# Optimization experiments

Hardware: AMD Instinct MI355X
Metric: run time of the kernel (lower is better)

Reference implementation:

```python
import jax, jax.numpy as jnp
import numpy as np

NUM_EDGE_TYPES = 8
HIDDEN = 128
N_NODES = 50000
N_EDGES = 600000


def setup_inputs() -> dict:
    key = jax.random.key(0)
    ks = jax.random.split(key, 10)
    H = HIDDEN
    h = jax.random.normal(ks[0], (N_NODES, H), dtype=jnp.float32)
    edge_index = jax.random.randint(ks[1], (2, N_EDGES), 0, N_NODES, dtype=jnp.int32)
    edge_type = jax.random.randint(ks[2], (N_EDGES,), 0, NUM_EDGE_TYPES + 1, dtype=jnp.int32)
    s = 1.0 / np.sqrt(H)
    W_msg = jax.random.uniform(ks[3], (H, H), jnp.float32, -s, s)
    b_msg = jax.random.uniform(ks[4], (H,), jnp.float32, -s, s)
    edge_embed = jax.random.normal(ks[5], (NUM_EDGE_TYPES + 1, H), dtype=jnp.float32)
    W_ih = jax.random.uniform(ks[6], (3 * H, H), jnp.float32, -s, s)
    W_hh = jax.random.uniform(ks[7], (3 * H, H), jnp.float32, -s, s)
    b_ih = jax.random.uniform(ks[8], (3 * H,), jnp.float32, -s, s)
    b_hh = jax.random.uniform(ks[9], (3 * H,), jnp.float32, -s, s)
    return {"h": h, "edge_index": edge_index, "edge_type": edge_type,
            "num_nodes": N_NODES, "W_msg": W_msg, "b_msg": b_msg,
            "edge_embed": edge_embed, "W_ih": W_ih, "W_hh": W_hh,
            "b_ih": b_ih, "b_hh": b_hh}


def _gru_cell(x, h, W_ih, W_hh, b_ih, b_hh):
    # PyTorch GRUCell: gates ordered (r, z, n)
    H = h.shape[-1]
    gi = x @ W_ih.T + b_ih  # (N, 3H)
    gh = h @ W_hh.T + b_hh
    i_r, i_z, i_n = gi[:, :H], gi[:, H:2 * H], gi[:, 2 * H:]
    h_r, h_z, h_n = gh[:, :H], gh[:, H:2 * H], gh[:, 2 * H:]
    r = jax.nn.sigmoid(i_r + h_r)
    z = jax.nn.sigmoid(i_z + h_z)
    n = jnp.tanh(i_n + r * h_n)
    return (1.0 - z) * n + z * h


def reference(h, edge_index, edge_type, num_nodes, W_msg, b_msg, edge_embed, W_ih, W_hh, b_ih, b_hh):
    src = edge_index[0]
    dst = edge_index[1]
    # gather -> linear -> edge-type embed add
    src_h = h[src] @ W_msg.T + b_msg                      # (E, H)
    emb = edge_embed[jnp.clip(edge_type, 0, NUM_EDGE_TYPES)]  # (E, H)
    msg = src_h + emb
    # scatter-add into per-node message buffer
    messages = jax.ops.segment_sum(msg, dst, num_segments=num_nodes)  # (num_nodes, H)
    h_new = _gru_cell(messages, h[:num_nodes], W_ih, W_hh, b_ih, b_hh)
    result = jnp.zeros_like(h).at[:num_nodes].set(h_new)
    return result
```

## Files before the change

### kernel.cpp

```cpp
#include <hip/hip_runtime.h>
#include <math.h>

#define H 128
typedef unsigned int u32;
typedef unsigned long long u64;
typedef __attribute__((ext_vector_type(8))) short short8;
typedef __attribute__((ext_vector_type(4))) float floatx4;

#define XS_STRIDE 136
#define CS_STRIDE 40
#define CAP 64

__device__ __forceinline__ float sigmoid_f(float x) {
    return 1.0f / (1.0f + __expf(-x));
}
__device__ __forceinline__ float tanh_f(float x) {
    float t = __expf(-2.0f * fabsf(x));
    float r = (1.0f - t) / (1.0f + t);
    return copysignf(r, x);
}
__device__ __forceinline__ unsigned short f2bf(float x) {
    u32 u = __float_as_uint(x);
    return (unsigned short)((u + 0x7fffu + ((u >> 16) & 1u)) >> 16);
}
__device__ __forceinline__ float bf2f(unsigned short s) {
    return __uint_as_float(((u32)s) << 16);
}
__device__ __forceinline__ float bf_lo32(u32 u) { return __uint_as_float(u << 16); }
__device__ __forceinline__ float bf_hi32(u32 u) { return __uint_as_float(u & 0xffff0000u); }

__global__ __launch_bounds__(256) void fused_pre_kernel(
    const float* __restrict__ h, unsigned short* __restrict__ h_b, int total8,
    int* __restrict__ deg, int* __restrict__ ohead, int N,
    const float* __restrict__ Wih, const float* __restrict__ Whh,
    const float* __restrict__ Wm,  const float* __restrict__ emb,
    const float* __restrict__ bm,
    unsigned short* __restrict__ Wcs, unsigned short* __restrict__ Whhs,
    unsigned short* __restrict__ embWs, int HB, int DB)
{
    int b = blockIdx.x;
    if (b < HB) {
        int idx = b * 256 + threadIdx.x;
        if (idx >= total8) return;
        const float4* p = (const float4*)(h + (size_t)idx * 8);
        float4 a = p[0], bb = p[1];
        short8 v;
        v[0] = (short)f2bf(a.x);  v[1] = (short)f2bf(a.y);
        v[2] = (short)f2bf(a.z);  v[3] = (short)f2bf(a.w);
        v[4] = (short)f2bf(bb.x); v[5] = (short)f2bf(bb.y);
        v[6] = (short)f2bf(bb.z); v[7] = (short)f2bf(bb.w);
        *(short8*)(h_b + (size_t)idx * 8) = v;
        return;
    }
    if (b < HB + DB) {
        int idx = (b - HB) * 256 + threadIdx.x;
        if (idx < N) deg[idx] = 0;
        else if (idx < 2 * N) ohead[idx - N] = -1;
        return;
    }
    int idx = (b - HB - DB) * 256 + threadIdx.x;
    if (idx < 49152) {
        int g = idx >> 7;
        int k = idx & 127;
        float acc = 0.f;
#pragma unroll 4
        for (int c = 0; c < H; ++c)
            acc += Wih[(size_t)g * H + c] * Wm[(size_t)c * H + k];
        int gate = g >> 7;
        int wi = g & 127;
        int j = wi >> 4, m = wi & 15;
        int kc = k >> 5, q = (k >> 3) & 3, i = k & 7;
        int l = q * 16 + m;
        Wcs[(size_t)(((gate * 8 + j) * 4 + kc) * 64 + l) * 8 + i] = f2bf(acc);
    } else if (idx < 61440) {
        int s = idx - 49152;
        int i = s & 7;
        int l = (s >> 3) & 63;
        int jb = s >> 9;
        int gate = jb >> 3, jj = jb & 7;
        int q = l >> 4, m = l & 15;
        int t = q * 8 + i;
        unsigned short v = 0;
        if (t < 9) {
            int g = gate * 128 + jj * 16 + m;
            float acc = 0.f;
#pragma unroll 4
            for (int jx = 0; jx < H; ++jx)
                acc += (emb[(size_t)t * H + jx] + bm[jx]) * Wih[(size_t)g * H + jx];
            v = f2bf(acc);
        }
        embWs[s] = v;
    } else if (idx < 67584) {
        int t2 = idx - 61440;
        int l  = t2 & 63;
        int kc = (t2 >> 6) & 3;
        int jr = t2 >> 8;
        int m = l & 15, q = l >> 4;
        size_t srco = (size_t)(jr * 16 + m) * H + kc * 32 + q * 8;
        const float4* s0 = (const float4*)(Whh + srco);
        float4 a = s0[0], bb = s0[1];
        short8 v;
        v[0] = (short)f2bf(a.x);  v[1] = (short)f2bf(a.y);
        v[2] = (short)f2bf(a.z);  v[3] = (short)f2bf(a.w);
        v[4] = (short)f2bf(bb.x); v[5] = (short)f2bf(bb.y);
        v[6] = (short)f2bf(bb.z); v[7] = (short)f2bf(bb.w);
        *(short8*)(Whhs + (size_t)t2 * 8) = v;
    }
}

__global__ __launch_bounds__(256) void fill_bucket_kernel(
    const int* __restrict__ eidx, const int* __restrict__ etype,
    int* __restrict__ deg, int* __restrict__ slots,
    int* __restrict__ ohead, int* __restrict__ onext,
    int* __restrict__ packed, int E)
{
    int e = blockIdx.x * 256 + threadIdx.x;
    if (e >= E) return;
    int src = eidx[e];
    int dst = eidx[E + e];
    int t = etype[e];
    t = t < 0 ? 0 : (t > 8 ? 8 : t);
    int enc = src | (t << 24);
    int p = atomicAdd(&deg[dst], 1);
    if (p < CAP) {
        slots[(size_t)dst * CAP + p] = enc;
    } else {
        packed[e] = enc;
        int old = atomicExch(&ohead[dst], e);
        onext[e] = old;
    }
}

__global__ __launch_bounds__(256) void gather_bucket_kernel(
    const unsigned short* __restrict__ h_b,
    const int* __restrict__ deg, const int* __restrict__ slots,
    const int* __restrict__ ohead, const int* __restrict__ onext,
    const int* __restrict__ packed,
    unsigned short* __restrict__ S_b, u64* __restrict__ cnt, int N)
{
    int n = blockIdx.x * 4 + (threadIdx.x >> 6);
    if (n >= N) return;
    int lane = threadIdx.x & 63;
    int dcnt = deg[n];
    int m = dcnt < CAP ? dcnt : CAP;
    const int* row = slots + (size_t)n * CAP;

    float ax = 0.f, ay = 0.f;
    u64 c = 0;
    int i = 0;
    for (; i + 8 <= m; i += 8) {
        int u0 = row[i + 0];
        int u1 = row[i + 1];
        int u2 = row[i + 2];
        int u3 = row[i + 3];
        int u4 = row[i + 4];
        int u5 = row[i + 5];
        int u6 = row[i + 6];
        int u7 = row[i + 7];
        u32 x0 = *((const u32*)(h_b + (size_t)(u0 & 0xffffff) * H) + lane);
        u32 x1 = *((const u32*)(h_b + (size_t)(u1 & 0xffffff) * H) + lane);
        u32 x2 = *((const u32*)(h_b + (size_t)(u2 & 0xffffff) * H) + lane);
        u32 x3 = *((const u32*)(h_b + (size_t)(u3 & 0xffffff) * H) + lane);
        u32 x4 = *((const u32*)(h_b + (size_t)(u4 & 0xffffff) * H) + lane);
        u32 x5 = *((const u32*)(h_b + (size_t)(u5 & 0xffffff) * H) + lane);
        u32 x6 = *((const u32*)(h_b + (size_t)(u6 & 0xffffff) * H) + lane);
        u32 x7 = *((const u32*)(h_b + (size_t)(u7 & 0xffffff) * H) + lane);
        c += (1ull << (7 * (u0 >> 24))) + (1ull << (7 * (u1 >> 24)))
           + (1ull << (7 * (u2 >> 24))) + (1ull << (7 * (u3 >> 24)))
           + (1ull << (7 * (u4 >> 24))) + (1ull << (7 * (u5 >> 24)))
           + (1ull << (7 * (u6 >> 24))) + (1ull << (7 * (u7 >> 24)));
        ax += bf_lo32(x0) + bf_lo32(x1) + bf_lo32(x2) + bf_lo32(x3)
            + bf_lo32(x4) + bf_lo32(x5) + bf_lo32(x6) + bf_lo32(x7);
        ay += bf_hi32(x0) + bf_hi32(x1) + bf_hi32(x2) + bf_hi32(x3)
            + bf_hi32(x4) + bf_hi32(x5) + bf_hi32(x6) + bf_hi32(x7);
    }
    for (; i + 4 <= m; i += 4) {
        int u0 = row[i + 0];
        int u1 = row[i + 1];
        int u2 = row[i + 2];
        int u3 = row[i + 3];
        u32 x0 = *((const u32*)(h_b + (size_t)(u0 & 0xffffff) * H) + lane);
        u32 x1 = *((const u32*)(h_b + (size_t)(u1 & 0xffffff) * H) + lane);
        u32 x2 = *((const u32*)(h_b + (size_t)(u2 & 0xffffff) * H) + lane);
        u32 x3 = *((const u32*)(h_b + (size_t)(u3 & 0xffffff) * H) + lane);
        c += (1ull << (7 * (u0 >> 24))) + (1ull << (7 * (u1 >> 24)))
           + (1ull << (7 * (u2 >> 24))) + (1ull << (7 * (u3 >> 24)));
        ax += bf_lo32(x0) + bf_lo32(x1) + bf_lo32(x2) + bf_lo32(x3);
        ay += bf_hi32(x0) + bf_hi32(x1) + bf_hi32(x2) + bf_hi32(x3);
    }
    for (; i < m; ++i) {
        int u = row[i];
        u32 x = *((const u32*)(h_b + (size_t)(u & 0xffffff) * H) + lane);
        c += 1ull << (7 * (u >> 24));
        ax += bf_lo32(x);
        ay += bf_hi32(x);
    }
    if (dcnt > CAP) {
        int ecur = ohead[n];
        while (ecur >= 0) {
            int u = packed[ecur];
            u32 x = *((const u32*)(h_b + (size_t)(u & 0xffffff) * H) + lane);
            c += 1ull << (7 * (u >> 24));
            ax += bf_lo32(x);
            ay += bf_hi32(x);
            ecur = onext[ecur];
        }
    }
    u32 o = (u32)f2bf(ax) | ((u32)f2bf(ay) << 16);
    *((u32*)(S_b + (size_t)n * H) + lane) = o;
    if (lane == 0) cnt[n] = c;
}

__global__ __launch_bounds__(256, 4) void gru_mfma_kernel(
    const unsigned short* __restrict__ S_b, const unsigned short* __restrict__ h_b,
    const unsigned short* __restrict__ Wcs, const unsigned short* __restrict__ Whhs,
    const unsigned short* __restrict__ embWs,
    const float* __restrict__ bih, const float* __restrict__ bhh,
    const u64* __restrict__ cnt,
    const int* __restrict__ numn, float* __restrict__ out, int N)
{
    __shared__ unsigned short xs[64 * XS_STRIDE];
    __shared__ unsigned short hsb[64 * XS_STRIDE];
    __shared__ unsigned short cs[64 * CS_STRIDE];

    int tid = threadIdx.x;
    int bx = blockIdx.x;
    int node0 = (bx >> 1) * 64;
    int jhalf = bx & 1;

    int lane = tid & 63;
    int wv = tid >> 6;
    int j = jhalf * 4 + wv;

    short8 er = *(const short8*)(embWs + (size_t)((0 * 8 + j) * 64 + lane) * 8);
    short8 ez = *(const short8*)(embWs + (size_t)((1 * 8 + j) * 64 + lane) * 8);
    short8 en = *(const short8*)(embWs + (size_t)((2 * 8 + j) * 64 + lane) * 8);

    for (int c = tid; c < 1024; c += 256) {
        int r = c >> 4;
        int k8 = (c & 15) << 3;
        int n = node0 + r;
        int nc = n < N ? n : N - 1;
        *(short8*)(&xs[r * XS_STRIDE + k8]) =
            *(const short8*)(S_b + (size_t)nc * H + k8);
        *(short8*)(&hsb[r * XS_STRIDE + k8]) =
            *(const short8*)(h_b + (size_t)nc * H + k8);
    }
    {
        int r = tid >> 2, tg = tid & 3;
        int n = node0 + r;
        u64 cv = cnt[n < N ? n : N - 1];
        short8 v = {0, 0, 0, 0, 0, 0, 0, 0};
        if (tg == 0) {
#pragma unroll
            for (int i = 0; i < 8; ++i)
                v[i] = (short)f2bf((float)((u32)(cv >> (7 * i)) & 127u));
        } else if (tg == 1) {
            v[0] = (short)f2bf((float)((u32)(cv >> 56) & 127u));
        }
        *(short8*)(&cs[r * CS_STRIDE + tg * 8]) = v;
    }
    __syncthreads();

    int am = lane & 15;
    int aq = lane >> 4;

    int num_nodes = numn[0];
    floatx4 zero = {0.f, 0.f, 0.f, 0.f};

    floatx4 aR[4], aZ[4], aIn[4], aHn[4];
#pragma unroll
    for (int rt = 0; rt < 4; ++rt) {
        short8 acn = *(const short8*)(&cs[(rt * 16 + am) * CS_STRIDE + aq * 8]);
        aR[rt]  = __builtin_amdgcn_mfma_f32_16x16x32_bf16(acn, er, zero, 0, 0, 0);
        aZ[rt]  = __builtin_amdgcn_mfma_f32_16x16x32_bf16(acn, ez, zero, 0, 0, 0);
        aIn[rt] = __builtin_amdgcn_mfma_f32_16x16x32_bf16(acn, en, zero, 0, 0, 0);
        aHn[rt] = zero;
    }
#pragma unroll
    for (int kc = 0; kc < 4; ++kc) {
        size_t c_r = (size_t)(((0 * 8 + j) * 4 + kc) * 64 + lane) * 8;
        size_t c_z = (size_t)(((1 * 8 + j) * 4 + kc) * 64 + lane) * 8;
        size_t c_n = (size_t)(((2 * 8 + j) * 4 + kc) * 64 + lane) * 8;
        short8 bir = *(const short8*)(Wcs + c_r);
        short8 bhr = *(const short8*)(Whhs + c_r);
        short8 biz = *(const short8*)(Wcs + c_z);
        short8 bhz = *(const short8*)(Whhs + c_z);
        short8 bin = *(const short8*)(Wcs + c_n);
        short8 bhn = *(const short8*)(Whhs + c_n);
#pragma unroll
        for (int rt = 0; rt < 4; ++rt) {
            int arow = rt * 16 + am;
            short8 axv = *(const short8*)(&xs[arow * XS_STRIDE + kc * 32 + aq * 8]);
            short8 ahv = *(const short8*)(&hsb[arow * XS_STRIDE + kc * 32 + aq * 8]);
            aR[rt]  = __builtin_amdgcn_mfma_f32_16x16x32_bf16(axv, bir, aR[rt], 0, 0, 0);
            aR[rt]  = __builtin_amdgcn_mfma_f32_16x16x32_bf16(ahv, bhr, aR[rt], 0, 0, 0);
            aZ[rt]  = __builtin_amdgcn_mfma_f32_16x16x32_bf16(axv, biz, aZ[rt], 0, 0, 0);
            aZ[rt]  = __builtin_amdgcn_mfma_f32_16x16x32_bf16(ahv, bhz, aZ[rt], 0, 0, 0);
            aIn[rt] = __builtin_amdgcn_mfma_f32_16x16x32_bf16(axv, bin, aIn[rt], 0, 0, 0);
            aHn[rt] = __builtin_amdgcn_mfma_f32_16x16x32_bf16(ahv, bhn, aHn[rt], 0, 0, 0);
        }
    }
    int c = j * 16 + am;
    float b_r = bih[c]       + bhh[c];
    float b_z = bih[128 + c] + bhh[128 + c];
    float b_in = bih[256 + c], b_hn = bhh[256 + c];
#pragma unroll
    for (int rt = 0; rt < 4; ++rt) {
#pragma unroll
        for (int q = 0; q < 4; ++q) {
            int m = rt * 16 + aq * 4 + q;
            int node = node0 + m;
            if (node < N) {
                float r  = sigmoid_f(aR[rt][q] + b_r);
                float z  = sigmoid_f(aZ[rt][q] + b_z);
                float nv = tanh_f((aIn[rt][q] + b_in) + r * (aHn[rt][q] + b_hn));
                float hv = bf2f(hsb[m * XS_STRIDE + c]);
                float o  = (1.0f - z) * nv + z * hv;
                out[(size_t)node * H + c] = (node < num_nodes) ? o : 0.0f;
            }
        }
    }
}

extern "C" void kernel_launch(void* const* d_in, const int* in_sizes, int n_in,
                              void* d_out, int out_size, void* d_ws, size_t ws_size,
                              hipStream_t stream) {
    const float* h    = (const float*)d_in[0];
    const int*  eidx  = (const int*)d_in[1];
    const int*  etype = (const int*)d_in[2];
    const int*  numn  = (const int*)d_in[3];
    const float* Wm   = (const float*)d_in[4];
    const float* bm   = (const float*)d_in[5];
    const float* emb  = (const float*)d_in[6];
    const float* Wih  = (const float*)d_in[7];
    const float* Whh  = (const float*)d_in[8];
    const float* bih  = (const float*)d_in[9];
    const float* bhh  = (const float*)d_in[10];

    int N = in_sizes[0] / H;
    int E = in_sizes[2];

    unsigned short* S_b   = (unsigned short*)d_ws;
    unsigned short* h_b   = S_b + (size_t)N * H;
    unsigned short* Wcs   = h_b + (size_t)N * H;
    unsigned short* Whhs  = Wcs + 3 * H * H;
    unsigned short* embWs = Whhs + 3 * H * H;
    u64* cnt    = (u64*)(embWs + 12288);
    int* deg    = (int*)(cnt + N);
    int* ohead  = deg + N;
    int* slots  = ohead + N;
    int* packed = slots + (size_t)N * CAP;
    int* onext  = packed + E;

    int total8 = N * H / 8;
    int HB = (total8 + 255) / 256;
    int DB = (2 * N + 255) / 256;
    int PB = 264;
    fused_pre_kernel<<<HB + DB + PB, 256, 0, stream>>>(
        h, h_b, total8, deg, ohead, N, Wih, Whh, Wm, emb, bm, Wcs, Whhs, embWs,
        HB, DB);

    fill_bucket_kernel<<<(E + 255) / 256, 256, 0, stream>>>(
        eidx, etype, deg, slots, ohead, onext, packed, E);

    gather_bucket_kernel<<<(N + 3) / 4, 256, 0, stream>>>(
        h_b, deg, slots, ohead, onext, packed, S_b, cnt, N);

    int nblk = ((N + 63) / 64) * 2;
    gru_mfma_kernel<<<nblk, 256, 0, stream>>>(S_b, h_b, Wcs, Whhs, embWs,
                                              bih, bhh, cnt, numn, (float*)d_out, N);
}
```

Measured before the change: 194.7 us.

## Replace per-node atomic slot buckets with binned two-pass CSR build

Edges are first binned into coarse buckets of 256 destination nodes, each split into 8 sub-bins, so global atomics land on far fewer counters. A new per-bucket kernel then builds a compact CSR in shared memory with a local histogram and prefix scan. The gather reads a dense packed row per node instead of a sparse 64-slot row. This adds one kernel launch and an extra pass over the edge records in exchange for fewer contended global atomics and more compact edge lists.

```diff
diff --git a/kernel.cpp b/kernel.cpp
--- a/kernel.cpp
+++ b/kernel.cpp
@@ -9,7 +9,9 @@
 
 #define XS_STRIDE 136
 #define CS_STRIDE 40
-#define CAP 64
+#define SBCAP 640
+#define NSUB 8
+#define BUCKCAP (SBCAP * NSUB)
 
 __device__ __forceinline__ float sigmoid_f(float x) {
     return 1.0f / (1.0f + __expf(-x));
@@ -31,7 +33,7 @@
 
 __global__ __launch_bounds__(256) void fused_pre_kernel(
     const float* __restrict__ h, unsigned short* __restrict__ h_b, int total8,
-    int* __restrict__ deg, int* __restrict__ ohead, int N,
+    int* __restrict__ ohead, int* __restrict__ bcnt, int N, int NS,
     const float* __restrict__ Wih, const float* __restrict__ Whh,
     const float* __restrict__ Wm,  const float* __restrict__ emb,
     const float* __restrict__ bm,
@@ -54,8 +56,8 @@
     }
     if (b < HB + DB) {
         int idx = (b - HB) * 256 + threadIdx.x;
-        if (idx < N) deg[idx] = 0;
-        else if (idx < 2 * N) ohead[idx - N] = -1;
+        if (idx < N) ohead[idx] = -1;
+        else if (idx < N + NS) bcnt[idx - N] = 0;
         return;
     }
     int idx = (b - HB - DB) * 256 + threadIdx.x;
@@ -108,11 +110,11 @@
     }
 }
 
-__global__ __launch_bounds__(256) void fill_bucket_kernel(
+__global__ __launch_bounds__(256) void fill_bin_kernel(
     const int* __restrict__ eidx, const int* __restrict__ etype,
-    int* __restrict__ deg, int* __restrict__ slots,
-    int* __restrict__ ohead, int* __restrict__ onext,
-    int* __restrict__ packed, int E)
+    int* __restrict__ bcnt, u64* __restrict__ brec,
+    int* __restrict__ ohead, int* __restrict__ onext, int* __restrict__ opk,
+    int E)
 {
     int e = blockIdx.x * 256 + threadIdx.x;
     if (e >= E) return;
@@ -120,30 +122,95 @@
     int dst = eidx[E + e];
     int t = etype[e];
     t = t < 0 ? 0 : (t > 8 ? 8 : t);
-    int enc = src | (t << 24);
-    int p = atomicAdd(&deg[dst], 1);
-    if (p < CAP) {
-        slots[(size_t)dst * CAP + p] = enc;
+    int ctr = (dst >> 8) * NSUB + (e & (NSUB - 1));
+    int p = atomicAdd(&bcnt[ctr], 1);
+    if (p < SBCAP) {
+        brec[(size_t)ctr * SBCAP + p] =
+            ((u64)(u32)src << 16) | ((u64)t << 8) | (u64)(dst & 255);
     } else {
-        packed[e] = enc;
+        opk[e] = src | (t << 24);
         int old = atomicExch(&ohead[dst], e);
         onext[e] = old;
     }
 }
 
-__global__ __launch_bounds__(256) void gather_bucket_kernel(
+__global__ __launch_bounds__(256) void csr_kernel(
+    const u64* __restrict__ brec, const int* __restrict__ bcnt,
+    int* __restrict__ deg, int* __restrict__ start,
+    int* __restrict__ packed, int N)
+{
+    __shared__ u64 recs[BUCKCAP];
+    __shared__ int ldeg[256];
+    __shared__ int lscan[256];
+    __shared__ int lpos[256];
+
+    int b = blockIdx.x;
+    int tid = threadIdx.x;
+    int n0 = b << 8;
+
+    int c[NSUB], base[NSUB];
+    int tot = 0;
+#pragma unroll
+    for (int s = 0; s < NSUB; ++s) {
+        int cc = bcnt[b * NSUB + s];
+        cc = cc < SBCAP ? cc : SBCAP;
+        c[s] = cc;
+        base[s] = tot;
+        tot += cc;
+    }
+#pragma unroll
+    for (int s = 0; s < NSUB; ++s) {
+        const u64* srcp = brec + (size_t)(b * NSUB + s) * SBCAP;
+        for (int i = tid; i < c[s]; i += 256) recs[base[s] + i] = srcp[i];
+    }
+    ldeg[tid] = 0;
+    __syncthreads();
+
+    for (int i = tid; i < tot; i += 256)
+        atomicAdd(&ldeg[(u32)recs[i] & 255u], 1);
+    __syncthreads();
+
+    lscan[tid] = ldeg[tid];
+    __syncthreads();
+    for (int d = 1; d < 256; d <<= 1) {
+        int v = (tid >= d) ? lscan[tid - d] : 0;
+        __syncthreads();
+        lscan[tid] += v;
+        __syncthreads();
+    }
+    int st = lscan[tid] - ldeg[tid];
+    lpos[tid] = st;
+    int n = n0 + tid;
+    int gbase = b * BUCKCAP;
+    if (n < N) {
+        deg[n] = ldeg[tid];
+        start[n] = gbase + st;
+    }
+    __syncthreads();
+
+    for (int i = tid; i < tot; i += 256) {
+        u64 r = recs[i];
+        int d = (u32)r & 255u;
+        int t = ((u32)r >> 8) & 255u;
+        int src = (int)(r >> 16);
+        int p = atomicAdd(&lpos[d], 1);
+        packed[gbase + p] = src | (t << 24);
+    }
+}
+
+__global__ __launch_bounds__(256) void gather_csr_kernel(
     const unsigned short* __restrict__ h_b,
-    const int* __restrict__ deg, const int* __restrict__ slots,
+    const int* __restrict__ deg, const int* __restrict__ start,
+    const int* __restrict__ packed,
     const int* __restrict__ ohead, const int* __restrict__ onext,
-    const int* __restrict__ packed,
+    const int* __restrict__ opk,
     unsigned short* __restrict__ S_b, u64* __restrict__ cnt, int N)
 {
     int n = blockIdx.x * 4 + (threadIdx.x >> 6);
     if (n >= N) return;
     int lane = threadIdx.x & 63;
-    int dcnt = deg[n];
-    int m = dcnt < CAP ? dcnt : CAP;
-    const int* row = slots + (size_t)n * CAP;
+    int m = deg[n];
+    const int* row = packed + start[n];
 
     float ax = 0.f, ay = 0.f;
     u64 c = 0;
@@ -195,10 +262,11 @@
         ax += bf_lo32(x);
         ay += bf_hi32(x);
     }
-    if (dcnt > CAP) {
-        int ecur = ohead[n];
+    int oh = ohead[n];
+    if (oh >= 0) {
+        int ecur = oh;
         while (ecur >= 0) {
-            int u = packed[ecur];
+            int u = opk[ecur];
             u32 x = *((const u32*)(h_b + (size_t)(u & 0xffffff) * H) + lane);
             c += 1ull << (7 * (u >> 24));
             ax += bf_lo32(x);
@@ -340,6 +408,8 @@
 
     int N = in_sizes[0] / H;
     int E = in_sizes[2];
+    int NB = (N + 255) >> 8;
+    int NS = NB * NSUB;
 
     unsigned short* S_b   = (unsigned short*)d_ws;
     unsigned short* h_b   = S_b + (size_t)N * H;
@@ -348,24 +418,29 @@
     unsigned short* embWs = Whhs + 3 * H * H;
     u64* cnt    = (u64*)(embWs + 12288);
     int* deg    = (int*)(cnt + N);
-    int* ohead  = deg + N;
-    int* slots  = ohead + N;
-    int* packed = slots + (size_t)N * CAP;
-    int* onext  = packed + E;
+    int* start  = deg + N;
+    int* ohead  = start + N;
+    int* bcnt   = ohead + N;
+    u64* brec   = (u64*)(bcnt + ((NS + 1) & ~1));
+    int* packed = (int*)(brec + (size_t)NS * SBCAP);
+    int* onext  = packed + (size_t)NB * BUCKCAP;
+    int* opk    = onext + E;
 
     int total8 = N * H / 8;
     int HB = (total8 + 255) / 256;
-    int DB = (2 * N + 255) / 256;
+    int DB = (N + NS + 255) / 256;
     int PB = 264;
     fused_pre_kernel<<<HB + DB + PB, 256, 0, stream>>>(
-        h, h_b, total8, deg, ohead, N, Wih, Whh, Wm, emb, bm, Wcs, Whhs, embWs,
-        HB, DB);
-
-    fill_bucket_kernel<<<(E + 255) / 256, 256, 0, stream>>>(
-        eidx, etype, deg, slots, ohead, onext, packed, E);
-
-    gather_bucket_kernel<<<(N + 3) / 4, 256, 0, stream>>>(
-        h_b, deg, slots, ohead, onext, packed, S_b, cnt, N);
+        h, h_b, total8, ohead, bcnt, N, NS, Wih, Whh, Wm, emb, bm,
+        Wcs, Whhs, embWs, HB, DB);
+
+    fill_bin_kernel<<<(E + 255) / 256, 256, 0, stream>>>(
+        eidx, etype, bcnt, brec, ohead, onext, opk, E);
+
+    csr_kernel<<<NB, 256, 0, stream>>>(brec, bcnt, deg, start, packed, N);
+
+    gather_csr_kernel<<<(N + 3) / 4, 256, 0, stream>>>(
+        h_b, deg, start, packed, ohead, onext, opk, S_b, cnt, N);
 
     int nblk = ((N + 63) / 64) * 2;
     gru_mfma_kernel<<<nblk, 256, 0, stream>>>(S_b, h_b, Wcs, Whhs, embWs,
```

After: 266.4 us. 36.9% more time.

## Replace atomic-count bucket fill with per-node linked lists compacted to CSR rows

Applied to the files above, without the earlier changes.

Edge binning now pushes each edge onto one of four per-destination linked lists with atomicExch, replacing the atomicAdd slot allocation. A new kernel walks the four chains per node, staging up to 32 entries each in shared memory, then writes them as a contiguous row of up to 128 and records the degree. Overflow entries are relinked into a per-node overflow list that the gather kernel still handles. This trades contended atomicAdd plus slot writes for cheaper exchanges and an extra pointer-chasing launch with serialized chain walks.

```diff
diff --git a/kernel.cpp b/kernel.cpp
--- a/kernel.cpp
+++ b/kernel.cpp
@@ -9,7 +9,7 @@
 
 #define XS_STRIDE 136
 #define CS_STRIDE 40
-#define CAP 64
+#define ROWCAP 128
 
 __device__ __forceinline__ float sigmoid_f(float x) {
     return 1.0f / (1.0f + __expf(-x));
@@ -31,7 +31,7 @@
 
 __global__ __launch_bounds__(256) void fused_pre_kernel(
     const float* __restrict__ h, unsigned short* __restrict__ h_b, int total8,
-    int* __restrict__ deg, int* __restrict__ ohead, int N,
+    int* __restrict__ head4, int* __restrict__ ohead, int N,
     const float* __restrict__ Wih, const float* __restrict__ Whh,
     const float* __restrict__ Wm,  const float* __restrict__ emb,
     const float* __restrict__ bm,
@@ -54,8 +54,8 @@
     }
     if (b < HB + DB) {
         int idx = (b - HB) * 256 + threadIdx.x;
-        if (idx < N) deg[idx] = 0;
-        else if (idx < 2 * N) ohead[idx - N] = -1;
+        if (idx < 4 * N) head4[idx] = -1;
+        else if (idx < 5 * N) ohead[idx - 4 * N] = -1;
         return;
     }
     int idx = (b - HB - DB) * 256 + threadIdx.x;
@@ -108,10 +108,9 @@
     }
 }
 
-__global__ __launch_bounds__(256) void fill_bucket_kernel(
+__global__ __launch_bounds__(256) void fill_ll_kernel(
     const int* __restrict__ eidx, const int* __restrict__ etype,
-    int* __restrict__ deg, int* __restrict__ slots,
-    int* __restrict__ ohead, int* __restrict__ onext,
+    int* __restrict__ head4, int* __restrict__ nexte,
     int* __restrict__ packed, int E)
 {
     int e = blockIdx.x * 256 + threadIdx.x;
@@ -120,30 +119,66 @@
     int dst = eidx[E + e];
     int t = etype[e];
     t = t < 0 ? 0 : (t > 8 ? 8 : t);
-    int enc = src | (t << 24);
-    int p = atomicAdd(&deg[dst], 1);
-    if (p < CAP) {
-        slots[(size_t)dst * CAP + p] = enc;
-    } else {
-        packed[e] = enc;
-        int old = atomicExch(&ohead[dst], e);
-        onext[e] = old;
-    }
-}
-
-__global__ __launch_bounds__(256) void gather_bucket_kernel(
+    packed[e] = src | (t << 24);
+    int old = atomicExch(&head4[(size_t)dst * 4 + (e & 3)], e);
+    nexte[e] = old;
+}
+
+__global__ __launch_bounds__(256) void ll2csr_kernel(
+    const int* __restrict__ head4, int* __restrict__ nexte,
+    const int* __restrict__ packed,
+    int* __restrict__ slots, int* __restrict__ deg,
+    int* __restrict__ ohead, int N)
+{
+    __shared__ int lbuf[256 * 33];
+
+    int tid = threadIdx.x;
+    int lane = tid & 63;
+    int wv = tid >> 6;
+    int n = (blockIdx.x * 4 + wv) * 16 + (lane >> 2);
+    int cchain = lane & 3;
+    bool valid = n < N;
+
+    int e = valid ? head4[(size_t)n * 4 + cchain] : -1;
+    int cnt = 0;
+    int lbase = tid * 33;
+    while (e >= 0) {
+        int nx = nexte[e];
+        int u = packed[e];
+        if (cnt < 32) {
+            lbuf[lbase + cnt] = u;
+        } else {
+            nexte[e] = atomicExch(&ohead[n], e);
+        }
+        cnt++;
+        e = nx;
+    }
+    int cl = cnt < 32 ? cnt : 32;
+    int base = lane & ~3;
+    int c0 = __shfl(cl, base);
+    int c1 = __shfl(cl, base + 1);
+    int c2 = __shfl(cl, base + 2);
+    int c3 = __shfl(cl, base + 3);
+    int pc = (cchain > 0 ? c0 : 0) + (cchain > 1 ? c1 : 0) + (cchain > 2 ? c2 : 0);
+    if (valid) {
+        int* drow = slots + (size_t)n * ROWCAP + pc;
+        for (int i = 0; i < cl; ++i) drow[i] = lbuf[lbase + i];
+        if (cchain == 0) deg[n] = c0 + c1 + c2 + c3;
+    }
+}
+
+__global__ __launch_bounds__(256) void gather_csr_kernel(
     const unsigned short* __restrict__ h_b,
     const int* __restrict__ deg, const int* __restrict__ slots,
-    const int* __restrict__ ohead, const int* __restrict__ onext,
+    const int* __restrict__ ohead, const int* __restrict__ nexte,
     const int* __restrict__ packed,
     unsigned short* __restrict__ S_b, u64* __restrict__ cnt, int N)
 {
     int n = blockIdx.x * 4 + (threadIdx.x >> 6);
     if (n >= N) return;
     int lane = threadIdx.x & 63;
-    int dcnt = deg[n];
-    int m = dcnt < CAP ? dcnt : CAP;
-    const int* row = slots + (size_t)n * CAP;
+    int m = deg[n];
+    const int* row = slots + (size_t)n * ROWCAP;
 
     float ax = 0.f, ay = 0.f;
     u64 c = 0;
@@ -195,15 +230,16 @@
         ax += bf_lo32(x);
         ay += bf_hi32(x);
     }
-    if (dcnt > CAP) {
-        int ecur = ohead[n];
+    int oh = ohead[n];
+    if (oh >= 0) {
+        int ecur = oh;
         while (ecur >= 0) {
             int u = packed[ecur];
             u32 x = *((const u32*)(h_b + (size_t)(u & 0xffffff) * H) + lane);
             c += 1ull << (7 * (u >> 24));
             ax += bf_lo32(x);
             ay += bf_hi32(x);
-            ecur = onext[ecur];
+            ecur = nexte[ecur];
         }
     }
     u32 o = (u32)f2bf(ax) | ((u32)f2bf(ay) << 16);
@@ -349,23 +385,27 @@
     u64* cnt    = (u64*)(embWs + 12288);
     int* deg    = (int*)(cnt + N);
     int* ohead  = deg + N;
-    int* slots  = ohead + N;
-    int* packed = slots + (size_t)N * CAP;
-    int* onext  = packed + E;
+    int* head4  = ohead + N;
+    int* slots  = head4 + 4 * N;
+    int* packed = slots + (size_t)N * ROWCAP;
+    int* nexte  = packed + E;
 
     int total8 = N * H / 8;
     int HB = (total8 + 255) / 256;
-    int DB = (2 * N + 255) / 256;
+    int DB = (5 * N + 255) / 256;
     int PB = 264;
     fused_pre_kernel<<<HB + DB + PB, 256, 0, stream>>>(
-        h, h_b, total8, deg, ohead, N, Wih, Whh, Wm, emb, bm, Wcs, Whhs, embWs,
-        HB, DB);
-
-    fill_bucket_kernel<<<(E + 255) / 256, 256, 0, stream>>>(
-        eidx, etype, deg, slots, ohead, onext, packed, E);
-
-    gather_bucket_kernel<<<(N + 3) / 4, 256, 0, stream>>>(
-        h_b, deg, slots, ohead, onext, packed, S_b, cnt, N);
+        h, h_b, total8, head4, ohead, N, Wih, Whh, Wm, emb, bm,
+        Wcs, Whhs, embWs, HB, DB);
+
+    fill_ll_kernel<<<(E + 255) / 256, 256, 0, stream>>>(
+        eidx, etype, head4, nexte, packed, E);
+
+    ll2csr_kernel<<<(N + 63) / 64, 256, 0, stream>>>(
+        head4, nexte, packed, slots, deg, ohead, N);
+
+    gather_csr_kernel<<<(N + 3) / 4, 256, 0, stream>>>(
+        h_b, deg, slots, ohead, nexte, packed, S_b, cnt, N);
 
     int nblk = ((N + 63) / 64) * 2;
     gru_mfma_kernel<<<nblk, 256, 0, stream>>>(S_b, h_b, Wcs, Whhs, embWs,
```

New measurement: 206.3 us. +6.0%, slower.
